# Performance work log

Hardware: AMD Instinct MI355X
Metric: run time of the kernel (lower is better)

The kernel has to match this reference:

```python
import jax, jax.numpy as jnp
import numpy as np

WS = 7       # window size
SHIFT = 3    # shift size (ws//2)
NH = 16      # num heads
DIM = 512    # channels
HH = 112
WW = 112
HIDDEN = int(DIM * 4.0)
EPS = 1e-5


def _rel_index():
    # Swin relative position index, [N, N] ints into the bias table
    coords = np.stack(np.meshgrid(np.arange(WS), np.arange(WS), indexing='ij')).reshape(2, -1)
    rel = coords[:, :, None] - coords[:, None, :]
    rel = rel.transpose(1, 2, 0) + (WS - 1)
    rel[:, :, 0] *= 2 * WS - 1
    return rel.sum(-1)


def _attn_mask():
    # shifted-window mask on HH x WW (already multiples of WS) -> [nW, N, N] with 0 / -1e9
    img = np.zeros((HH, WW), np.int32)
    cnt = 0
    sl = (slice(0, -WS), slice(-WS, -SHIFT), slice(-SHIFT, None))
    for h in sl:
        for w in sl:
            img[h, w] = cnt
            cnt += 1
    win = img.reshape(HH // WS, WS, WW // WS, WS).transpose(0, 2, 1, 3).reshape(-1, WS * WS)
    diff = win[:, None, :] - win[:, :, None]
    return np.where(diff == 0, 0.0, -1e9).astype(np.float32)


def setup_inputs() -> dict:
    key = jax.random.key(0)
    ks = jax.random.split(key, 8)
    s = 0.02
    return {
        'x': jax.random.normal(ks[0], (DIM, HH, WW), jnp.float32),
        'norm1_w': jnp.ones((DIM,), jnp.float32),
        'norm1_b': jnp.zeros((DIM,), jnp.float32),
        'qkv_w': jax.random.normal(ks[1], (3 * DIM, DIM), jnp.float32) * s,
        'qkv_b': jnp.zeros((3 * DIM,), jnp.float32),
        'proj_w': jax.random.normal(ks[2], (DIM, DIM), jnp.float32) * s,
        'proj_b': jnp.zeros((DIM,), jnp.float32),
        'rpb_table': jax.random.normal(ks[3], ((2 * WS - 1) ** 2, NH), jnp.float32) * s,
        'norm2_w': jnp.ones((DIM,), jnp.float32),
        'norm2_b': jnp.zeros((DIM,), jnp.float32),
        'fc1_w': jax.random.normal(ks[4], (HIDDEN, DIM), jnp.float32) * s,
        'fc1_b': jnp.zeros((HIDDEN,), jnp.float32),
        'fc2_w': jax.random.normal(ks[5], (DIM, HIDDEN), jnp.float32) * s,
        'fc2_b': jnp.zeros((DIM,), jnp.float32),
    }


def _ln(x_hwc, w, b):
    m = x_hwc.mean(-1, keepdims=True)
    v = x_hwc.var(-1, keepdims=True)
    return (x_hwc - m) / jnp.sqrt(v + EPS) * w + b


def reference(x, norm1_w, norm1_b, qkv_w, qkv_b, proj_w, proj_b, rpb_table,
              norm2_w, norm2_b, fc1_w, fc1_b, fc2_w, fc2_b):
    C, H, W = x.shape
    ws = WS
    N = ws * ws
    hd = C // NH
    scale = 1.0 / np.sqrt(hd).astype(np.float32)

    x_hwc = jnp.moveaxis(x, 0, -1)                       # [H,W,C]
    xn = _ln(x_hwc, norm1_w, norm1_b)
    xs = jnp.roll(xn, (-SHIFT, -SHIFT), (0, 1))          # cyclic shift
    # window partition -> [nW, N, C]
    xw = xs.reshape(H // ws, ws, W // ws, ws, C).transpose(0, 2, 1, 3, 4).reshape(-1, N, C)

    qkv = xw @ qkv_w.T + qkv_b                            # [nW,N,3C]
    q, k, v = jnp.split(qkv, 3, -1)
    heads = lambda t: t.reshape(-1, N, NH, hd).transpose(0, 2, 1, 3)  # [nW,H,N,hd]
    q, k, v = heads(q), heads(k), heads(v)

    attn = jnp.einsum('whnd,whmd->whnm', q * scale, k)    # [nW,H,N,N]
    idx = jnp.asarray(_rel_index().reshape(-1))
    bias = rpb_table[idx].reshape(N, N, NH).transpose(2, 0, 1)  # [H,N,N]
    mask = jnp.asarray(_attn_mask())                       # [nW,N,N]
    attn = attn + bias[None] + mask[:, None]
    attn = jax.nn.softmax(attn, -1)

    out = jnp.einsum('whnm,whmd->whnd', attn, v).transpose(0, 2, 1, 3).reshape(-1, N, C)
    out = out @ proj_w.T + proj_b
    # window unpartition + reverse shift
    out = out.reshape(H // ws, W // ws, ws, ws, C).transpose(0, 2, 1, 3, 4).reshape(H, W, C)
    out = jnp.roll(out, (SHIFT, SHIFT), (0, 1))

    x1 = x_hwc + out                                       # residual (DropPath rate 0)
    x2 = _ln(x1, norm2_w, norm2_b)
    h = jax.nn.gelu(x2.reshape(-1, C) @ fc1_w.T + fc1_b)
    m = (h @ fc2_w.T + fc2_b).reshape(H, W, C)
    y = x1 + m
    return jnp.moveaxis(y, -1, 0)                          # back to [C,H,W]
```

## Files before the change

kernel.cpp:

```cpp
#include <hip/hip_runtime.h>

#define NPIX 12544
#define CDIM 512
#define QKVN 1536
#define HIDDEN 2048

typedef unsigned short u16;
typedef unsigned int u32;

typedef short bf16x8 __attribute__((ext_vector_type(8)));
typedef float f32x4 __attribute__((ext_vector_type(4)));

static __device__ __forceinline__ u16 f2bf(float f) {
  u32 u = __float_as_uint(f);
  return (u16)((u + 0x7fffu + ((u >> 16) & 1u)) >> 16);
}
static __device__ __forceinline__ u32 pack2(float a, float b) {
  return (u32)f2bf(a) | ((u32)f2bf(b) << 16);
}
static __device__ __forceinline__ u32 packtrunc2(float lo, float hi) {
  return __builtin_amdgcn_perm(__float_as_uint(hi), __float_as_uint(lo), 0x07060302u);
}
static __device__ __forceinline__ void async_ld16(const void* g, void* l) {
  __builtin_amdgcn_global_load_lds((__attribute__((address_space(1))) void*)g,
                                   (__attribute__((address_space(3))) void*)l, 16, 0, 0);
}

__global__ __launch_bounds__(256) void convert_weights(
    const float* __restrict__ qw, const float* __restrict__ pw,
    const float* __restrict__ w1, const float* __restrict__ w2,
    u16* __restrict__ Wq, u16* __restrict__ Wp, u16* __restrict__ W1o, u16* __restrict__ W2o) {
  const int b = blockIdx.x;
  const float* src; u16* dst; long off;
  if (b < 768)       { src = qw; dst = Wq;  off = (long)b * 1024; }
  else if (b < 1024) { src = pw; dst = Wp;  off = (long)(b - 768) * 1024; }
  else if (b < 2048) { src = w1; dst = W1o; off = (long)(b - 1024) * 1024; }
  else               { src = w2; dst = W2o; off = (long)(b - 2048) * 1024; }
  const long i = off / 4 + threadIdx.x;
  const float4 v = ((const float4*)src)[i];
  ushort4 u;
  u.x = f2bf(v.x); u.y = f2bf(v.y); u.z = f2bf(v.z); u.w = f2bf(v.w);
  ((ushort4*)dst)[i] = u;
}

__global__ __launch_bounds__(256) void ln1_partial(const float* __restrict__ x,
                                                   float* __restrict__ psum, float* __restrict__ pssq) {
  const int p = blockIdx.x * 256 + threadIdx.x;
  const int c0 = blockIdx.y * 32;
  float s = 0.f, ss = 0.f;
#pragma unroll
  for (int c = 0; c < 32; c++) {
    const float v = x[(long)(c0 + c) * NPIX + p];
    s += v; ss += v * v;
  }
  psum[blockIdx.y * NPIX + p] = s;
  pssq[blockIdx.y * NPIX + p] = ss;
}

__global__ __launch_bounds__(256) void ln1_stats(const float* __restrict__ psum, const float* __restrict__ pssq,
                                                 float* __restrict__ mean, float* __restrict__ rstd) {
  const int p = blockIdx.x * 256 + threadIdx.x;
  float s = 0.f, ss = 0.f;
#pragma unroll
  for (int ch = 0; ch < 16; ch++) { s += psum[ch * NPIX + p]; ss += pssq[ch * NPIX + p]; }
  const float m = s * (1.f / 512.f);
  const float v = ss * (1.f / 512.f) - m * m;
  mean[p] = m;
  rstd[p] = rsqrtf(v + 1e-5f);
}

__global__ __launch_bounds__(256) void ln1_shift_part(const float* __restrict__ x,
    const float* __restrict__ mean, const float* __restrict__ rstd,
    const float* __restrict__ gw, const float* __restrict__ gb, u16* __restrict__ xw) {
  __shared__ float tile[32][65];
  const int p0 = blockIdx.x * 64;
  const int c0 = blockIdx.y * 32;
  const int t = threadIdx.x;
  {
    const int pl = t & 63;
    const int cl0 = t >> 6;
#pragma unroll
    for (int r = 0; r < 8; r++) {
      const int cl = r * 4 + cl0;
      tile[cl][pl] = x[(long)(c0 + cl) * NPIX + p0 + pl];
    }
  }
  __syncthreads();
  const int cl = t & 31;
  const int g = t >> 5;
  const float wc = gw[c0 + cl];
  const float bc = gb[c0 + cl];
#pragma unroll
  for (int pass = 0; pass < 8; pass++) {
    const int pl = pass * 8 + g;
    const int p = p0 + pl;
    const int h = p / 112;
    const int w = p - h * 112;
    int hs = h + 109; if (hs >= 112) hs -= 112;
    int ws2 = w + 109; if (ws2 >= 112) ws2 -= 112;
    const int hq = hs / 7, wq = ws2 / 7;
    const int tok = (hq * 16 + wq) * 49 + (hs - hq * 7) * 7 + (ws2 - wq * 7);
    const float val = (tile[cl][pl] - mean[p]) * rstd[p] * wc + bc;
    xw[(long)tok * 512 + c0 + cl] = f2bf(val);
  }
}

template<bool OUT_BF16, bool DO_GELU, bool REMAP, bool FUSE_Y>
__global__ __launch_bounds__(256, 3) void gemm_bt(
    const u16* __restrict__ A, const u16* __restrict__ B,
    const float* __restrict__ bias, void* __restrict__ out,
    const float* __restrict__ x1, const int N, const int K) {
  __shared__ __align__(16) u16 Asm[128 * 64];
  __shared__ __align__(16) u16 Bsm[128 * 64];
  const int M0 = blockIdx.x << 7;
  const int N0 = blockIdx.y << 7;
  const int t = threadIdx.x;
  const int wave = t >> 6;
  const int lane = t & 63;
  const int l15 = lane & 15;
  const int quad = lane >> 4;
  const int wm = wave & 1;
  const int wn = wave >> 1;
  const int swz8 = l15 & 7;

  f32x4 acc[4][4] = {};

  for (int k0 = 0; k0 < K; k0 += 64) {
#pragma unroll
    for (int i = 0; i < 4; i++) {
      const int flatbase = i * 256 + wave * 64;
      const int FL = flatbase + lane;
      const int row = FL >> 3;
      const int c = (FL & 7) ^ (row & 7);
      async_ld16(A + (long)(M0 + row) * K + k0 + c * 8, Asm + flatbase * 8);
      async_ld16(B + (long)(N0 + row) * K + k0 + c * 8, Bsm + flatbase * 8);
    }
    __syncthreads();
#pragma unroll
    for (int ks = 0; ks < 2; ks++) {
      bf16x8 af[4], bfr[4];
#pragma unroll
      for (int im = 0; im < 4; im++)
        af[im] = *(const bf16x8*)&Asm[(wm * 64 + im * 16 + l15) * 64 + ((ks * 4 + quad) ^ swz8) * 8];
#pragma unroll
      for (int in = 0; in < 4; in++)
        bfr[in] = *(const bf16x8*)&Bsm[(wn * 64 + in * 16 + l15) * 64 + ((ks * 4 + quad) ^ swz8) * 8];
#pragma unroll
      for (int im = 0; im < 4; im++)
#pragma unroll
        for (int in = 0; in < 4; in++)
          acc[im][in] = __builtin_amdgcn_mfma_f32_16x16x32_bf16(bfr[in], af[im], acc[im][in], 0, 0, 0);
    }
    __syncthreads();
  }

#pragma unroll
  for (int im = 0; im < 4; im++) {
    const int row = M0 + wm * 64 + im * 16 + l15;
    long orow = row;
    if (REMAP) {
      const int win = row / 49;
      const int nn = row - win * 49;
      const int nq = nn / 7;
      const int hs = (win >> 4) * 7 + nq;
      const int wsx = (win & 15) * 7 + (nn - nq * 7);
      int h = hs + 3; if (h >= 112) h -= 112;
      int w = wsx + 3; if (w >= 112) w -= 112;
      orow = h * 112 + w;
    }
#pragma unroll
    for (int in = 0; in < 4; in++) {
      const int col0 = N0 + wn * 64 + in * 16 + quad * 4;
      const float4 bv = *(const float4*)(bias + col0);
      float v[4];
      if (FUSE_Y) {
        const float4 xv = *(const float4*)(x1 + (long)row * CDIM + col0);
#pragma unroll
        for (int r = 0; r < 4; r++)
          v[r] = acc[im][in][r] + ((const float*)&bv)[r] + ((const float*)&xv)[r];
#pragma unroll
        for (int r = 0; r < 4; r++)
          ((float*)out)[(long)(col0 + r) * NPIX + row] = v[r];
      } else {
#pragma unroll
        for (int r = 0; r < 4; r++) {
          float vv = acc[im][in][r] + ((const float*)&bv)[r];
          if (DO_GELU) {
            const float z2 = 1.5957691216f * (vv + 0.044715f * vv * vv * vv);
            vv = vv / (1.0f + __expf(-z2));
          }
          v[r] = vv;
        }
        if (OUT_BF16) {
          uint2 u;
          u.x = pack2(v[0], v[1]);
          u.y = pack2(v[2], v[3]);
          *(uint2*)((u16*)out + orow * (long)N + col0) = u;
        } else {
          float4 f; f.x = v[0]; f.y = v[1]; f.z = v[2]; f.w = v[3];
          *(float4*)((float*)out + orow * (long)N + col0) = f;
        }
      }
    }
  }
}

__global__ __launch_bounds__(256) void build_biasT(const float* __restrict__ rpb, float* __restrict__ biasT) {
  const int cls = blockIdx.x >> 4;
  const int head = blockIdx.x & 15;
  for (int e = threadIdx.x; e < 4096; e += 256) {
    const int j = e >> 6;
    const int i = e & 63;
    float v;
    if (j >= 49) v = -1e9f;
    else if (i >= 49) v = 0.f;
    else {
      const int ri = i / 7, ci = i - (i / 7) * 7;
      const int rj = j / 7, cj = j - (j / 7) * 7;
      v = rpb[((ri - rj + 6) * 13 + (ci - cj + 6)) * 16 + head];
      const int lhi = (cls & 2) ? (ri < 4 ? 1 : 2) : 0;
      const int lwi = (cls & 1) ? (ci < 4 ? 1 : 2) : 0;
      const int lhj = (cls & 2) ? (rj < 4 ? 1 : 2) : 0;
      const int lwj = (cls & 1) ? (cj < 4 ? 1 : 2) : 0;
      if (lhi * 3 + lwi != lhj * 3 + lwj) v = -1e9f;
    }
    biasT[(long)blockIdx.x * 4096 + e] = v;
  }
}

__global__ __launch_bounds__(256, 3) void attn_mfma(
    const u16* __restrict__ qkv, const float* __restrict__ biasT, u16* __restrict__ out) {
  __shared__ __align__(16) u16 slds[24576];
  const int t = threadIdx.x;
  const int wave = t >> 6;
  const int lane = t & 63;
  const int l15 = lane & 15;
  const int quad = lane >> 4;
  const int win = blockIdx.x >> 2;
  const int head = (blockIdx.x & 3) * 4 + wave;
  const int cls = (((win >> 4) == 15) ? 2 : 0) | (((win & 15) == 15) ? 1 : 0);

  u16* Qb  = slds + wave * 6144;
  u16* Kb  = Qb + 2048;
  u16* Vtb = Qb + 4096;
  u16* Pb  = Qb;

  const int rrow = lane >> 2;
  const int chunk = (lane & 3) ^ ((lane >> 3) & 3);
  uint4 vv[4];
#pragma unroll
  for (int it = 0; it < 4; it++) {
    const int row = it * 16 + rrow;
    const int jc = row < 49 ? row : 48;
    const long gbase = (long)(win * 49 + jc) * 1536 + head * 32 + chunk * 8;
    async_ld16(qkv + gbase,       Qb + it * 512 + lane * 8);
    async_ld16(qkv + gbase + 512, Kb + it * 512 + lane * 8);
    vv[it] = *(const uint4*)(qkv + gbase + 1024);
  }
  __syncthreads();

#pragma unroll
  for (int it = 0; it < 4; it++) {
    const int row = it * 16 + rrow;
    const u32* w = (const u32*)&vv[it];
#pragma unroll
    for (int tt = 0; tt < 8; tt++) {
      const int d = chunk * 8 + tt;
      const u16 val = (tt & 1) ? (u16)(w[tt >> 1] >> 16) : (u16)(w[tt >> 1] & 0xffffu);
      Vtb[d * 64 + (row ^ (((d >> 2) & 3) << 4))] = val;
    }
  }

  const int fswz = (l15 >> 1) & 3;
  bf16x8 kfrag[4], qfrag[4];
#pragma unroll
  for (int jm = 0; jm < 4; jm++)
    kfrag[jm] = *(const bf16x8*)(Kb + (jm * 16 + l15) * 32 + (quad ^ fswz) * 8);
#pragma unroll
  for (int in = 0; in < 4; in++)
    qfrag[in] = *(const bf16x8*)(Qb + (in * 16 + l15) * 32 + (quad ^ fswz) * 8);
  f32x4 sacc[4][4] = {};
#pragma unroll
  for (int jm = 0; jm < 4; jm++)
#pragma unroll
    for (int in = 0; in < 4; in++)
      sacc[jm][in] = __builtin_amdgcn_mfma_f32_16x16x32_bf16(kfrag[jm], qfrag[in], sacc[jm][in], 0, 0, 0);

  const float* bT = biasT + (long)(cls * 16 + head) * 4096;
  const float sc = 0.17677669529663687f;
#pragma unroll
  for (int jm = 0; jm < 4; jm++) {
    const float* bp = bT + (jm * 16 + quad * 4) * 64 + l15;
#pragma unroll
    for (int in = 0; in < 4; in++)
#pragma unroll
      for (int r = 0; r < 4; r++)
        sacc[jm][in][r] = sacc[jm][in][r] * sc + bp[r * 64 + in * 16];
  }
  float linv[4];
#pragma unroll
  for (int in = 0; in < 4; in++) {
    float m = -1e30f;
#pragma unroll
    for (int jm = 0; jm < 4; jm++)
#pragma unroll
      for (int r = 0; r < 4; r++) m = fmaxf(m, sacc[jm][in][r]);
    m = fmaxf(m, __shfl_xor(m, 16));
    m = fmaxf(m, __shfl_xor(m, 32));
    float s = 0.f;
#pragma unroll
    for (int jm = 0; jm < 4; jm++)
#pragma unroll
      for (int r = 0; r < 4; r++) {
        const float e = __expf(sacc[jm][in][r] - m);
        sacc[jm][in][r] = e; s += e;
      }
    s += __shfl_xor(s, 16);
    s += __shfl_xor(s, 32);
    linv[in] = __builtin_amdgcn_rcpf(s);
  }

#pragma unroll
  for (int in = 0; in < 4; in++) {
    const int i = in * 16 + l15;
    const int rot = (l15 & 3) << 4;
#pragma unroll
    for (int jm = 0; jm < 4; jm++) {
      const u32 lo = packtrunc2(sacc[jm][in][0], sacc[jm][in][1]);
      const u32 hi = packtrunc2(sacc[jm][in][2], sacc[jm][in][3]);
      uint2 u; u.x = lo; u.y = hi;
      *(uint2*)(Pb + i * 64 + ((jm * 16 + quad * 4) ^ rot)) = u;
    }
  }

  f32x4 oacc[2][4] = {};
#pragma unroll
  for (int ks = 0; ks < 2; ks++) {
    bf16x8 vtf[2], pf[4];
#pragma unroll
    for (int dm = 0; dm < 2; dm++)
      vtf[dm] = *(const bf16x8*)(Vtb + (dm * 16 + l15) * 64 + ((ks * 32 + quad * 8) ^ ((l15 >> 2) << 4)));
#pragma unroll
    for (int in = 0; in < 4; in++)
      pf[in] = *(const bf16x8*)(Pb + (in * 16 + l15) * 64 + ((ks * 32 + quad * 8) ^ ((l15 & 3) << 4)));
#pragma unroll
    for (int dm = 0; dm < 2; dm++)
#pragma unroll
      for (int in = 0; in < 4; in++)
        oacc[dm][in] = __builtin_amdgcn_mfma_f32_16x16x32_bf16(vtf[dm], pf[in], oacc[dm][in], 0, 0, 0);
  }

#pragma unroll
  for (int in = 0; in < 4; in++) {
    const int i = in * 16 + l15;
    if (i < 49) {
      const float inv = linv[in];
      const long base = (long)(win * 49 + i) * 512 + head * 32 + quad * 4;
#pragma unroll
      for (int dm = 0; dm < 2; dm++) {
        const float v0 = oacc[dm][in][0] * inv, v1 = oacc[dm][in][1] * inv;
        const float v2 = oacc[dm][in][2] * inv, v3 = oacc[dm][in][3] * inv;
        uint2 u; u.x = packtrunc2(v0, v1); u.y = packtrunc2(v2, v3);
        *(uint2*)(out + base + dm * 16) = u;
      }
    }
  }
}

__global__ __launch_bounds__(256) void resid_kernel(const float* __restrict__ x,
    const float* __restrict__ proj, float* __restrict__ x1) {
  __shared__ float tile[32][65];
  const int p0 = blockIdx.x * 64;
  const int c0 = blockIdx.y * 32;
  const int t = threadIdx.x;
  {
    const int pl = t & 63;
    const int cl0 = t >> 6;
#pragma unroll
    for (int r = 0; r < 8; r++) {
      const int cl = r * 4 + cl0;
      tile[cl][pl] = x[(long)(c0 + cl) * NPIX + p0 + pl];
    }
  }
  __syncthreads();
  const int cl = t & 31;
  const int g = t >> 5;
#pragma unroll
  for (int pass = 0; pass < 8; pass++) {
    const int pl = pass * 8 + g;
    const long idx = (long)(p0 + pl) * 512 + c0 + cl;
    x1[idx] = tile[cl][pl] + proj[idx];
  }
}

__global__ __launch_bounds__(256) void ln2_apply(const float* __restrict__ x1,
    const float* __restrict__ gw, const float* __restrict__ gb, u16* __restrict__ x2) {
  const int wave = threadIdx.x >> 6;
  const int lane = threadIdx.x & 63;
  const int p = blockIdx.x * 4 + wave;
  const float4* row = (const float4*)(x1 + (long)p * 512);
  const float4 a = row[lane * 2];
  const float4 b = row[lane * 2 + 1];
  float s = a.x + a.y + a.z + a.w + b.x + b.y + b.z + b.w;
  float ss = a.x * a.x + a.y * a.y + a.z * a.z + a.w * a.w
           + b.x * b.x + b.y * b.y + b.z * b.z + b.w * b.w;
#pragma unroll
  for (int o = 32; o > 0; o >>= 1) { s += __shfl_xor(s, o); ss += __shfl_xor(ss, o); }
  const float m = s * (1.f / 512.f);
  const float var = ss * (1.f / 512.f) - m * m;
  const float rs = rsqrtf(var + 1e-5f);
  const float4 w0 = ((const float4*)gw)[lane * 2];
  const float4 w1 = ((const float4*)gw)[lane * 2 + 1];
  const float4 b0 = ((const float4*)gb)[lane * 2];
  const float4 b1 = ((const float4*)gb)[lane * 2 + 1];
  uint4 u;
  u.x = pack2((a.x - m) * rs * w0.x + b0.x, (a.y - m) * rs * w0.y + b0.y);
  u.y = pack2((a.z - m) * rs * w0.z + b0.z, (a.w - m) * rs * w0.w + b0.w);
  u.z = pack2((b.x - m) * rs * w1.x + b1.x, (b.y - m) * rs * w1.y + b1.y);
  u.w = pack2((b.z - m) * rs * w1.z + b1.z, (b.w - m) * rs * w1.w + b1.w);
  ((uint4*)(x2 + (long)p * 512))[lane] = u;
}

extern "C" void kernel_launch(void* const* d_in, const int* in_sizes, int n_in,
                              void* d_out, int out_size, void* d_ws, size_t ws_size,
                              hipStream_t stream) {
  (void)in_sizes; (void)n_in; (void)out_size; (void)ws_size;
  const float* x      = (const float*)d_in[0];
  const float* n1w    = (const float*)d_in[1];
  const float* n1b    = (const float*)d_in[2];
  const float* qkv_w  = (const float*)d_in[3];
  const float* qkv_b  = (const float*)d_in[4];
  const float* proj_w = (const float*)d_in[5];
  const float* proj_b = (const float*)d_in[6];
  const float* rpb    = (const float*)d_in[7];
  const float* n2w    = (const float*)d_in[8];
  const float* n2b    = (const float*)d_in[9];
  const float* fc1_w  = (const float*)d_in[10];
  const float* fc1_b  = (const float*)d_in[11];
  const float* fc2_w  = (const float*)d_in[12];
  const float* fc2_b  = (const float*)d_in[13];
  float* y = (float*)d_out;

  char* base = (char*)d_ws;
  size_t off = 0;
  auto alloc = [&](size_t b) { char* p = base + off; off += (b + 255) & ~(size_t)255; return p; };
  float* mean1 = (float*)alloc((size_t)NPIX * 4);
  float* rstd1 = (float*)alloc((size_t)NPIX * 4);
  float* psum  = (float*)alloc((size_t)16 * NPIX * 4);
  float* pssq  = (float*)alloc((size_t)16 * NPIX * 4);
  u16* Wq = (u16*)alloc((size_t)QKVN * CDIM * 2);
  u16* Wp = (u16*)alloc((size_t)CDIM * CDIM * 2);
  u16* W1 = (u16*)alloc((size_t)HIDDEN * CDIM * 2);
  u16* W2 = (u16*)alloc((size_t)CDIM * HIDDEN * 2);
  float* biasT = (float*)alloc((size_t)4 * 16 * 4096 * 4);
  u16* bufA = (u16*)alloc((size_t)NPIX * CDIM * 2);
  char* bufB = alloc((size_t)NPIX * QKVN * 2);
  float* x1 = (float*)alloc((size_t)NPIX * CDIM * 4);
  u16* hbuf = (u16*)alloc((size_t)NPIX * HIDDEN * 2);

  u16* xw      = bufA;
  u16* qkvbuf  = (u16*)bufB;
  u16* attnout = bufA;
  float* projout = (float*)bufB;
  u16* x2 = bufA;

  convert_weights<<<3072, 256, 0, stream>>>(qkv_w, proj_w, fc1_w, fc2_w, Wq, Wp, W1, W2);
  build_biasT<<<64, 256, 0, stream>>>(rpb, biasT);

  ln1_partial<<<dim3(49, 16), 256, 0, stream>>>(x, psum, pssq);
  ln1_stats<<<49, 256, 0, stream>>>(psum, pssq, mean1, rstd1);
  ln1_shift_part<<<dim3(196, 16), 256, 0, stream>>>(x, mean1, rstd1, n1w, n1b, xw);

  gemm_bt<true, false, false, false><<<dim3(98, QKVN / 128), 256, 0, stream>>>(xw, Wq, qkv_b, qkvbuf, nullptr, QKVN, CDIM);
  attn_mfma<<<1024, 256, 0, stream>>>(qkvbuf, biasT, attnout);
  gemm_bt<false, false, true, false><<<dim3(98, CDIM / 128), 256, 0, stream>>>(attnout, Wp, proj_b, projout, nullptr, CDIM, CDIM);

  resid_kernel<<<dim3(196, 16), 256, 0, stream>>>(x, projout, x1);
  ln2_apply<<<NPIX / 4, 256, 0, stream>>>(x1, n2w, n2b, x2);

  gemm_bt<true, true, false, false><<<dim3(98, HIDDEN / 128), 256, 0, stream>>>(x2, W1, fc1_b, hbuf, nullptr, HIDDEN, CDIM);
  gemm_bt<false, false, false, true><<<dim3(98, CDIM / 128), 256, 0, stream>>>(hbuf, W2, fc2_b, y, x1, CDIM, HIDDEN);
}
```

Baseline: 306.6 us.

## Double-buffer GEMM K-loop and fuse residual add into projection GEMM

```diff
diff --git a/kernel.cpp b/kernel.cpp
--- a/kernel.cpp
+++ b/kernel.cpp
@@ -105,13 +105,13 @@
   }
 }
 
-template<bool OUT_BF16, bool DO_GELU, bool REMAP, bool FUSE_Y>
+template<bool OUT_BF16, bool DO_GELU, bool REMAP, bool FUSE_Y, bool FUSE_X>
 __global__ __launch_bounds__(256, 3) void gemm_bt(
     const u16* __restrict__ A, const u16* __restrict__ B,
     const float* __restrict__ bias, void* __restrict__ out,
-    const float* __restrict__ x1, const int N, const int K) {
-  __shared__ __align__(16) u16 Asm[128 * 64];
-  __shared__ __align__(16) u16 Bsm[128 * 64];
+    const float* __restrict__ xtra, const int N, const int K) {
+  __shared__ __align__(16) u16 Asm[2][128 * 32];
+  __shared__ __align__(16) u16 Bsm[2][128 * 32];
   const int M0 = blockIdx.x << 7;
   const int N0 = blockIdx.y << 7;
   const int t = threadIdx.x;
@@ -121,37 +121,40 @@
   const int quad = lane >> 4;
   const int wm = wave & 1;
   const int wn = wave >> 1;
-  const int swz8 = l15 & 7;
-
-  f32x4 acc[4][4] = {};
-
-  for (int k0 = 0; k0 < K; k0 += 64) {
-#pragma unroll
-    for (int i = 0; i < 4; i++) {
+  const int swz = (l15 >> 1) & 3;
+
+  auto stage = [&](int k0, int b) {
+#pragma unroll
+    for (int i = 0; i < 2; i++) {
       const int flatbase = i * 256 + wave * 64;
       const int FL = flatbase + lane;
-      const int row = FL >> 3;
-      const int c = (FL & 7) ^ (row & 7);
-      async_ld16(A + (long)(M0 + row) * K + k0 + c * 8, Asm + flatbase * 8);
-      async_ld16(B + (long)(N0 + row) * K + k0 + c * 8, Bsm + flatbase * 8);
-    }
+      const int row = FL >> 2;
+      const int chunk = (FL & 3) ^ ((row >> 1) & 3);
+      async_ld16(A + (long)(M0 + row) * K + k0 + chunk * 8, &Asm[b][flatbase * 8]);
+      async_ld16(B + (long)(N0 + row) * K + k0 + chunk * 8, &Bsm[b][flatbase * 8]);
+    }
+  };
+
+  f32x4 acc[4][4] = {};
+  stage(0, 0);
+  int cur = 0;
+
+  for (int k0 = 0; k0 < K; k0 += 32) {
     __syncthreads();
-#pragma unroll
-    for (int ks = 0; ks < 2; ks++) {
-      bf16x8 af[4], bfr[4];
-#pragma unroll
-      for (int im = 0; im < 4; im++)
-        af[im] = *(const bf16x8*)&Asm[(wm * 64 + im * 16 + l15) * 64 + ((ks * 4 + quad) ^ swz8) * 8];
+    if (k0 + 32 < K) stage(k0 + 32, cur ^ 1);
+    bf16x8 af[4], bfr[4];
+#pragma unroll
+    for (int im = 0; im < 4; im++)
+      af[im] = *(const bf16x8*)&Asm[cur][(wm * 64 + im * 16 + l15) * 32 + (quad ^ swz) * 8];
+#pragma unroll
+    for (int in = 0; in < 4; in++)
+      bfr[in] = *(const bf16x8*)&Bsm[cur][(wn * 64 + in * 16 + l15) * 32 + (quad ^ swz) * 8];
+#pragma unroll
+    for (int im = 0; im < 4; im++)
 #pragma unroll
       for (int in = 0; in < 4; in++)
-        bfr[in] = *(const bf16x8*)&Bsm[(wn * 64 + in * 16 + l15) * 64 + ((ks * 4 + quad) ^ swz8) * 8];
-#pragma unroll
-      for (int im = 0; im < 4; im++)
-#pragma unroll
-        for (int in = 0; in < 4; in++)
-          acc[im][in] = __builtin_amdgcn_mfma_f32_16x16x32_bf16(bfr[in], af[im], acc[im][in], 0, 0, 0);
-    }
-    __syncthreads();
+        acc[im][in] = __builtin_amdgcn_mfma_f32_16x16x32_bf16(bfr[in], af[im], acc[im][in], 0, 0, 0);
+    cur ^= 1;
   }
 
 #pragma unroll
@@ -174,13 +177,20 @@
       const float4 bv = *(const float4*)(bias + col0);
       float v[4];
       if (FUSE_Y) {
-        const float4 xv = *(const float4*)(x1 + (long)row * CDIM + col0);
+        const float4 xv = *(const float4*)(xtra + (long)row * CDIM + col0);
 #pragma unroll
         for (int r = 0; r < 4; r++)
           v[r] = acc[im][in][r] + ((const float*)&bv)[r] + ((const float*)&xv)[r];
 #pragma unroll
         for (int r = 0; r < 4; r++)
           ((float*)out)[(long)(col0 + r) * NPIX + row] = v[r];
+      } else if (FUSE_X) {
+        float v0 = acc[im][in][0] + bv.x + xtra[(long)(col0 + 0) * NPIX + orow];
+        float v1 = acc[im][in][1] + bv.y + xtra[(long)(col0 + 1) * NPIX + orow];
+        float v2 = acc[im][in][2] + bv.z + xtra[(long)(col0 + 2) * NPIX + orow];
+        float v3 = acc[im][in][3] + bv.w + xtra[(long)(col0 + 3) * NPIX + orow];
+        float4 f; f.x = v0; f.y = v1; f.z = v2; f.w = v3;
+        *(float4*)((float*)out + orow * (long)N + col0) = f;
       } else {
 #pragma unroll
         for (int r = 0; r < 4; r++) {
@@ -364,32 +374,6 @@
         *(uint2*)(out + base + dm * 16) = u;
       }
     }
-  }
-}
-
-__global__ __launch_bounds__(256) void resid_kernel(const float* __restrict__ x,
-    const float* __restrict__ proj, float* __restrict__ x1) {
-  __shared__ float tile[32][65];
-  const int p0 = blockIdx.x * 64;
-  const int c0 = blockIdx.y * 32;
-  const int t = threadIdx.x;
-  {
-    const int pl = t & 63;
-    const int cl0 = t >> 6;
-#pragma unroll
-    for (int r = 0; r < 8; r++) {
-      const int cl = r * 4 + cl0;
-      tile[cl][pl] = x[(long)(c0 + cl) * NPIX + p0 + pl];
-    }
-  }
-  __syncthreads();
-  const int cl = t & 31;
-  const int g = t >> 5;
-#pragma unroll
-  for (int pass = 0; pass < 8; pass++) {
-    const int pl = pass * 8 + g;
-    const long idx = (long)(p0 + pl) * 512 + c0 + cl;
-    x1[idx] = tile[cl][pl] + proj[idx];
   }
 }
 
@@ -461,7 +445,6 @@
   u16* xw      = bufA;
   u16* qkvbuf  = (u16*)bufB;
   u16* attnout = bufA;
-  float* projout = (float*)bufB;
   u16* x2 = bufA;
 
   convert_weights<<<3072, 256, 0, stream>>>(qkv_w, proj_w, fc1_w, fc2_w, Wq, Wp, W1, W2);
@@ -471,13 +454,12 @@
   ln1_stats<<<49, 256, 0, stream>>>(psum, pssq, mean1, rstd1);
   ln1_shift_part<<<dim3(196, 16), 256, 0, stream>>>(x, mean1, rstd1, n1w, n1b, xw);
 
-  gemm_bt<true, false, false, false><<<dim3(98, QKVN / 128), 256, 0, stream>>>(xw, Wq, qkv_b, qkvbuf, nullptr, QKVN, CDIM);
+  gemm_bt<true, false, false, false, false><<<dim3(98, QKVN / 128), 256, 0, stream>>>(xw, Wq, qkv_b, qkvbuf, nullptr, QKVN, CDIM);
   attn_mfma<<<1024, 256, 0, stream>>>(qkvbuf, biasT, attnout);
-  gemm_bt<false, false, true, false><<<dim3(98, CDIM / 128), 256, 0, stream>>>(attnout, Wp, proj_b, projout, nullptr, CDIM, CDIM);
-
-  resid_kernel<<<dim3(196, 16), 256, 0, stream>>>(x, projout, x1);
+  gemm_bt<false, false, true, false, true><<<dim3(98, CDIM / 128), 256, 0, stream>>>(attnout, Wp, proj_b, x1, x, CDIM, CDIM);
+
   ln2_apply<<<NPIX / 4, 256, 0, stream>>>(x1, n2w, n2b, x2);
 
-  gemm_bt<true, true, false, false><<<dim3(98, HIDDEN / 128), 256, 0, stream>>>(x2, W1, fc1_b, hbuf, nullptr, HIDDEN, CDIM);
-  gemm_bt<false, false, false, true><<<dim3(98, CDIM / 128), 256, 0, stream>>>(hbuf, W2, fc2_b, y, x1, CDIM, HIDDEN);
-}
+  gemm_bt<true, true, false, false, false><<<dim3(98, HIDDEN / 128), 256, 0, stream>>>(x2, W1, fc1_b, hbuf, nullptr, HIDDEN, CDIM);
+  gemm_bt<false, false, false, true, false><<<dim3(98, CDIM / 128), 256, 0, stream>>>(hbuf, W2, fc2_b, y, x1, CDIM, HIDDEN);
+}
```

Measured after the change: 327.1 us. +6.7%, slower.
